# Kernel tuning notes

Measured on AMD Instinct MI355X. Metric: run time of the kernel, lower is better.

## Reference

```python
import math
import jax, jax.numpy as jnp
import numpy as np

B, C, NX, NY = 8, 16, 512, 512
N = 16384
N_RES, NH, S = 90, 5, 0.5


def _normal(x, mu, s):
    # exp(-0.5*((x-mu)/s)^2) / (sqrt(s^2) * sqrt(2*pi))  -- matches torch helper
    return jnp.exp(-0.5 * ((x - mu) / s) ** 2) / (jnp.sqrt(s * s) * math.sqrt(2.0 * math.pi))


def setup_inputs() -> dict:
    key = jax.random.key(0)
    k1, k2 = jax.random.split(key)
    x = jax.random.normal(k1, (B, C, NX, NY), dtype=jnp.float32)
    coords = jax.random.uniform(k2, (B, N, 2), dtype=jnp.float32)
    nh_m = (NH - 1) / 2 + 0.5
    pixel_offset_normal = jnp.linspace(nh_m, -nh_m, N_RES, dtype=jnp.float32)
    pixel_offset_indices = jnp.linspace(-(NH - 1) // 2, (NH - 1) // 2, NH, dtype=jnp.float32)
    s = jnp.float32(S)
    return {"x": x, "coords": coords, "s": s,
            "pixel_offset_normal": pixel_offset_normal,
            "pixel_offset_indices": pixel_offset_indices}


def reference(x, coords, s, pixel_offset_normal, pixel_offset_indices):
    b, n, _ = coords.shape
    _, c, nx, ny = x.shape
    nh = pixel_offset_indices.shape[0]

    # continuous positions in pixel space
    px = coords[:, :, 1] * (nx - 1)   # [b,n]
    py = coords[:, :, 0] * (ny - 1)
    rpx, rpy = jnp.round(px), jnp.round(py)

    # gaussian weights integrated over sub-pixel resolution (n_res samples -> nh bins)
    # NOTE: torch code clamps both axes with x.shape[-2] (=nx); replicated faithfully.
    pxo = jnp.clip(rpx[..., None] - pixel_offset_normal, 0.0, nx)   # [b,n,n_res]
    pyo = jnp.clip(rpy[..., None] - pixel_offset_normal, 0.0, nx)
    wx = _normal(pxo, px[..., None], s).reshape(b, n, nh, -1).sum(-1)  # [b,n,nh]
    wy = _normal(pyo, py[..., None], s).reshape(b, n, nh, -1).sum(-1)
    w2d = wx[..., :, None] * wy[..., None, :]                          # [b,n,nh,nh]
    w2d = w2d / w2d.reshape(b, n, -1).sum(-1)[..., None, None]

    # integer neighborhood indices (both axes clamped with nx-1, as in torch code)
    ix = jnp.clip(jnp.round(rpx[..., None] - pixel_offset_indices), 0, nx - 1).astype(jnp.int32)  # [b,n,nh]
    iy = jnp.clip(jnp.round(rpy[..., None] - pixel_offset_indices), 0, nx - 1).astype(jnp.int32)

    # per-batch gather of nh x nh neighborhoods (equivalent to torch's BxB gather + diagonal)
    flat = (ix[..., :, None] * ny + iy[..., None, :]).reshape(b, n * nh * nh)  # [b, n*nh*nh]
    xf = x.reshape(b, c, nx * ny)
    g = jax.vmap(lambda xi, idx: xi[:, idx])(xf, flat)       # [b,c,n*nh*nh]
    g = g.reshape(b, c, n, nh, nh)

    out = (g * w2d[:, None]).reshape(b, c, n, nh * nh).sum(-1)  # [b,c,n]
    return out
```

## Files before the change

kernel.cpp:

```cpp
#include <hip/hip_runtime.h>

#define BV    8
#define CV    16
#define NXV   512
#define NYV   512
#define NV    16384
#define NRES  90
#define NHV   5
#define TPB   256
#define CPERT 4

#define NPTS  (BV * NV)
#define TSH   3
#define TDIM  (NXV >> TSH)
#define NBUCKB (TDIM * TDIM)
#define NBUCK  (BV * NBUCKB)
#define SCANT 1024
#define SPT   (NBUCK / SCANT)

#if __has_builtin(__builtin_amdgcn_exp2f)
#define EXP2 __builtin_amdgcn_exp2f
#else
#define EXP2 exp2f
#endif

__global__ void zero_counts_kernel(int* __restrict__ counts) {
    int i = blockIdx.x * blockDim.x + threadIdx.x;
    if (i < NBUCK) counts[i] = 0;
}

__device__ __forceinline__ int bucket_key(float rpx, float rpy, int i) {
    const unsigned tx = ((unsigned)(int)rpx) >> TSH;
    const unsigned ty = ((unsigned)(int)rpy) >> TSH;
    unsigned m = 0;
    #pragma unroll
    for (int k = 0; k < 6; ++k)
        m |= (((tx >> k) & 1u) << (2 * k)) | (((ty >> k) & 1u) << (2 * k + 1));
    return (i >> 14) * NBUCKB + (int)m;
}

__global__ __launch_bounds__(TPB) void bucket_count_kernel(
    const float* __restrict__ coords, int* __restrict__ counts)
{
    const int i = blockIdx.x * TPB + threadIdx.x;
    const float2 cd = *(const float2*)(coords + (size_t)i * 2);
    const float rpx = rintf(cd.y * (float)(NXV - 1));
    const float rpy = rintf(cd.x * (float)(NYV - 1));
    atomicAdd(&counts[bucket_key(rpx, rpy, i)], 1);
}

__global__ __launch_bounds__(SCANT) void scan_kernel(
    const int* __restrict__ counts, int* __restrict__ cursors)
{
    __shared__ int sm[SCANT];
    const int tid  = threadIdx.x;
    const int base = tid * SPT;

    int v[SPT];
    int run = 0;
    #pragma unroll
    for (int k = 0; k < SPT; ++k) {
        v[k] = run;
        run += counts[base + k];
    }
    sm[tid] = run;
    __syncthreads();
    #pragma unroll
    for (int off = 1; off < SCANT; off <<= 1) {
        int t = sm[tid];
        if (tid >= off) t += sm[tid - off];
        __syncthreads();
        sm[tid] = t;
        __syncthreads();
    }
    const int tbase = sm[tid] - run;
    #pragma unroll
    for (int k = 0; k < SPT; ++k)
        cursors[base + k] = tbase + v[k];
}

__global__ __launch_bounds__(TPB) void scatter_weights_kernel(
    const float* __restrict__ coords,
    const float* __restrict__ s_ptr,
    const float* __restrict__ offn,
    const float* __restrict__ offi,
    int* __restrict__ cursors,
    float4* __restrict__ w8a, float4* __restrict__ w8b,
    float4* __restrict__ wx4, int4* __restrict__ off4,
    float4* __restrict__ misc)
{
    const int i = blockIdx.x * TPB + threadIdx.x;

    const float2 cd = *(const float2*)(coords + (size_t)i * 2);
    const float px  = cd.y * (float)(NXV - 1);
    const float py  = cd.x * (float)(NYV - 1);
    const float rpx = rintf(px);
    const float rpy = rintf(py);

    const int pos = atomicAdd(&cursors[bucket_key(rpx, rpy, i)], 1);

    const float s = s_ptr[0];
    const float k = -0.72134752044448169f / (s * s);

    float wx[NHV], wy[NHV];
    float sx = 0.f, sy = 0.f;
    #pragma unroll
    for (int h = 0; h < NHV; ++h) {
        float ax = 0.f, ay = 0.f;
        #pragma unroll 6
        for (int t = 0; t < NRES / NHV; ++t) {
            const float off = offn[h * (NRES / NHV) + t];
            const float vx = fminf(fmaxf(rpx - off, 0.f), (float)NXV);
            const float vy = fminf(fmaxf(rpy - off, 0.f), (float)NXV);
            const float dx = vx - px;
            const float dy = vy - py;
            ax += EXP2(k * dx * dx);
            ay += EXP2(k * dy * dy);
        }
        wx[h] = ax; wy[h] = ay;
        sx += ax;  sy += ay;
    }
    const float inv = 1.0f / (sx * sy);

    int ix[NHV], iy[NHV];
    #pragma unroll
    for (int h = 0; h < NHV; ++h) {
        const float fo = offi[h];
        ix[h] = (int)fminf(fmaxf(rintf(rpx - fo), 0.f), (float)(NXV - 1));
        iy[h] = (int)fminf(fmaxf(rintf(rpy - fo), 0.f), (float)(NXV - 1));
    }

    const int a = min(iy[NHV - 1] & ~3, NYV - 8);

    float w8[8];
    #pragma unroll
    for (int kk = 0; kk < 8; ++kk) {
        float w = 0.f;
        #pragma unroll
        for (int j = 0; j < NHV; ++j)
            w += (iy[j] - a == kk) ? wy[j] * inv : 0.f;
        w8[kk] = w;
    }

    w8a[pos] = make_float4(w8[0], w8[1], w8[2], w8[3]);
    w8b[pos] = make_float4(w8[4], w8[5], w8[6], w8[7]);
    wx4[pos] = make_float4(wx[0], wx[1], wx[2], wx[3]);
    off4[pos] = make_int4((ix[0] * NYV + a) * 4, (ix[1] * NYV + a) * 4,
                          (ix[2] * NYV + a) * 4, (ix[3] * NYV + a) * 4);
    misc[pos] = make_float4(wx[4], __int_as_float((ix[4] * NYV + a) * 4),
                            __int_as_float(i), 0.f);
}

__global__ __launch_bounds__(TPB, 4) void gather_kernel(
    const float* __restrict__ x,
    const float4* __restrict__ w8a, const float4* __restrict__ w8b,
    const float4* __restrict__ wx4, const int4* __restrict__ off4,
    const float4* __restrict__ misc,
    float* __restrict__ out)
{
    const int nwg = NPTS / TPB;
    const int bid = blockIdx.x;
    const int swz = (bid & 7) * (nwg / 8) + (bid >> 3);
    const int p   = swz * TPB + threadIdx.x;
    const int c0  = blockIdx.y * CPERT;

    const float4 wa = w8a[p];
    const float4 wb = w8b[p];
    const float4 wr = wx4[p];
    const int4   o4 = off4[p];
    const float4 ms = misc[p];
    const float  we = ms.x;
    const int    oe = __float_as_int(ms.y);
    const int    i  = __float_as_int(ms.z);
    const int    b  = i >> 14;
    const int    n  = i & (NV - 1);

    const int   ro[NHV] = {o4.x, o4.y, o4.z, o4.w, oe};
    const float rw[NHV] = {wr.x, wr.y, wr.z, wr.w, we};

    const char* base = (const char*)x + ((size_t)(b * CV + c0) << 20);
    float acc[CPERT];
    #pragma unroll
    for (int q = 0; q < CPERT; ++q) acc[q] = 0.f;

    #pragma unroll
    for (int q = 0; q < CPERT; ++q) {
        const char* bq = base + ((size_t)q << 20);
        #pragma unroll
        for (int r = 0; r < NHV; ++r) {
            const float4* rp = (const float4*)(bq + (size_t)(unsigned)ro[r]);
            const float4 va = rp[0];
            const float4 vb = rp[1];
            const float rs = va.x * wa.x + va.y * wa.y + va.z * wa.z +
                             va.w * wa.w + vb.x * wb.x + vb.y * wb.y +
                             vb.z * wb.z + vb.w * wb.w;
            acc[q] = fmaf(rw[r], rs, acc[q]);
        }
    }

    #pragma unroll
    for (int q = 0; q < CPERT; ++q)
        out[(((size_t)(b * CV + c0 + q)) << 14) + n] = acc[q];
}

extern "C" void kernel_launch(void* const* d_in, const int* in_sizes, int n_in,
                              void* d_out, int out_size, void* d_ws, size_t ws_size,
                              hipStream_t stream) {
    const float* x      = (const float*)d_in[0];
    const float* coords = (const float*)d_in[1];
    const float* s_ptr  = (const float*)d_in[2];
    const float* offn   = (const float*)d_in[3];
    const float* offi   = (const float*)d_in[4];
    float* out = (float*)d_out;

    char* w = (char*)d_ws;
    float4* w8a  = (float4*)w;  w += (size_t)NPTS * 16;
    float4* w8b  = (float4*)w;  w += (size_t)NPTS * 16;
    float4* wx4  = (float4*)w;  w += (size_t)NPTS * 16;
    int4*   off4 = (int4*)w;    w += (size_t)NPTS * 16;
    float4* misc = (float4*)w;  w += (size_t)NPTS * 16;
    int*    counts  = (int*)w;  w += (size_t)NBUCK * 4;
    int*    cursors = (int*)w;

    zero_counts_kernel<<<dim3(NBUCK / TPB), dim3(TPB), 0, stream>>>(counts);
    bucket_count_kernel<<<dim3(NPTS / TPB), dim3(TPB), 0, stream>>>(coords, counts);
    scan_kernel<<<dim3(1), dim3(SCANT), 0, stream>>>(counts, cursors);
    scatter_weights_kernel<<<dim3(NPTS / TPB), dim3(TPB), 0, stream>>>(
        coords, s_ptr, offn, offi, cursors, w8a, w8b, wx4, off4, misc);

    dim3 grid(NPTS / TPB, CV / CPERT, 1);
    gather_kernel<<<grid, dim3(TPB), 0, stream>>>(
        x, w8a, w8b, wx4, off4, misc, out);
}
```

Measured before the change: 287.9 us.

## Stage per-tile image patches in LDS and gather points from shared memory

Measured after the change: 262.2 us. -8.9%, faster.

```diff
diff --git a/kernel.cpp b/kernel.cpp
--- a/kernel.cpp
+++ b/kernel.cpp
@@ -8,16 +8,22 @@
 #define NRES  90
 #define NHV   5
 #define TPB   256
-#define CPERT 4
 
 #define NPTS  (BV * NV)
-#define TSH   3
+#define TSH   5
 #define TDIM  (NXV >> TSH)
 #define NBUCKB (TDIM * TDIM)
 #define NBUCK  (BV * NBUCKB)
 #define SCANT 1024
 #define SPT   (NBUCK / SCANT)
 
+#define CPG   4
+#define RROWS 36
+#define RCOLS 48
+#define RSEG  (RCOLS / 4)
+#define SLOTS_PER_CH (RROWS * RSEG)
+#define SLOTS (CPG * SLOTS_PER_CH)
+
 #if __has_builtin(__builtin_amdgcn_exp2f)
 #define EXP2 __builtin_amdgcn_exp2f
 #else
@@ -30,13 +36,9 @@
 }
 
 __device__ __forceinline__ int bucket_key(float rpx, float rpy, int i) {
-    const unsigned tx = ((unsigned)(int)rpx) >> TSH;
-    const unsigned ty = ((unsigned)(int)rpy) >> TSH;
-    unsigned m = 0;
-    #pragma unroll
-    for (int k = 0; k < 6; ++k)
-        m |= (((tx >> k) & 1u) << (2 * k)) | (((ty >> k) & 1u) << (2 * k + 1));
-    return (i >> 14) * NBUCKB + (int)m;
+    const int tr = ((int)rpx) >> TSH;
+    const int tc = ((int)rpy) >> TSH;
+    return (i >> 14) * NBUCKB + tr * TDIM + tc;
 }
 
 __global__ __launch_bounds__(TPB) void bucket_count_kernel(
@@ -50,7 +52,8 @@
 }
 
 __global__ __launch_bounds__(SCANT) void scan_kernel(
-    const int* __restrict__ counts, int* __restrict__ cursors)
+    const int* __restrict__ counts, int* __restrict__ starts,
+    int* __restrict__ cursors)
 {
     __shared__ int sm[SCANT];
     const int tid  = threadIdx.x;
@@ -75,8 +78,11 @@
     }
     const int tbase = sm[tid] - run;
     #pragma unroll
-    for (int k = 0; k < SPT; ++k)
-        cursors[base + k] = tbase + v[k];
+    for (int k = 0; k < SPT; ++k) {
+        const int e = tbase + v[k];
+        starts[base + k]  = e;
+        cursors[base + k] = e;
+    }
 }
 
 __global__ __launch_bounds__(TPB) void scatter_weights_kernel(
@@ -151,56 +157,81 @@
                             __int_as_float(i), 0.f);
 }
 
-__global__ __launch_bounds__(TPB, 4) void gather_kernel(
+__global__ __launch_bounds__(TPB) void tile_gather_kernel(
     const float* __restrict__ x,
+    const int* __restrict__ starts, const int* __restrict__ ends,
     const float4* __restrict__ w8a, const float4* __restrict__ w8b,
     const float4* __restrict__ wx4, const int4* __restrict__ off4,
     const float4* __restrict__ misc,
     float* __restrict__ out)
 {
-    const int nwg = NPTS / TPB;
+    __shared__ float4 lds[SLOTS];
+
     const int bid = blockIdx.x;
-    const int swz = (bid & 7) * (nwg / 8) + (bid >> 3);
-    const int p   = swz * TPB + threadIdx.x;
-    const int c0  = blockIdx.y * CPERT;
-
-    const float4 wa = w8a[p];
-    const float4 wb = w8b[p];
-    const float4 wr = wx4[p];
-    const int4   o4 = off4[p];
-    const float4 ms = misc[p];
-    const float  we = ms.x;
-    const int    oe = __float_as_int(ms.y);
-    const int    i  = __float_as_int(ms.z);
-    const int    b  = i >> 14;
-    const int    n  = i & (NV - 1);
-
-    const int   ro[NHV] = {o4.x, o4.y, o4.z, o4.w, oe};
-    const float rw[NHV] = {wr.x, wr.y, wr.z, wr.w, we};
-
-    const char* base = (const char*)x + ((size_t)(b * CV + c0) << 20);
-    float acc[CPERT];
-    #pragma unroll
-    for (int q = 0; q < CPERT; ++q) acc[q] = 0.f;
-
-    #pragma unroll
-    for (int q = 0; q < CPERT; ++q) {
-        const char* bq = base + ((size_t)q << 20);
-        #pragma unroll
-        for (int r = 0; r < NHV; ++r) {
-            const float4* rp = (const float4*)(bq + (size_t)(unsigned)ro[r]);
-            const float4 va = rp[0];
-            const float4 vb = rp[1];
-            const float rs = va.x * wa.x + va.y * wa.y + va.z * wa.z +
-                             va.w * wa.w + vb.x * wb.x + vb.y * wb.y +
-                             vb.z * wb.z + vb.w * wb.w;
-            acc[q] = fmaf(rw[r], rs, acc[q]);
+    const int cg  = blockIdx.y;
+    const int b   = bid >> 8;
+    const int tr  = (bid >> 4) & (TDIM - 1);
+    const int tc  = bid & (TDIM - 1);
+    const int r0  = tr << TSH, c0 = tc << TSH;
+    const int R0  = min(max(r0 - 2, 0), NXV - RROWS);
+    const int W0  = min(max(c0 - 8, 0), NYV - RCOLS);
+
+    const int tid = threadIdx.x;
+    const char* bx = (const char*)x + ((size_t)(b * CV + cg * CPG) << 20);
+
+    #pragma unroll
+    for (int kk = 0; kk < (SLOTS + TPB - 1) / TPB; ++kk) {
+        const int sslot = tid + kk * TPB;
+        if (sslot < SLOTS) {
+            const int ch  = sslot / SLOTS_PER_CH;
+            const int rem = sslot - ch * SLOTS_PER_CH;
+            const int row = rem / RSEG;
+            const int seg = rem - row * RSEG;
+            lds[sslot] = *(const float4*)(bx + ((size_t)ch << 20)
+                          + ((size_t)(R0 + row) << 11) + (W0 << 2) + (seg << 4));
         }
     }
-
-    #pragma unroll
-    for (int q = 0; q < CPERT; ++q)
-        out[(((size_t)(b * CV + c0 + q)) << 14) + n] = acc[q];
+    __syncthreads();
+
+    const int s0    = starts[bid];
+    const int total = (ends[bid] - s0) << 2;
+    const char* ldsb = (const char*)lds;
+
+    for (int item = tid; item < total; item += TPB) {
+        const int p  = s0 + (item >> 2);
+        const int ch = item & (CPG - 1);
+
+        const float4 wa = w8a[p];
+        const float4 wb = w8b[p];
+        const float4 wr = wx4[p];
+        const int4   o4 = off4[p];
+        const float4 ms = misc[p];
+        const float  we = ms.x;
+        const int    oe = __float_as_int(ms.y);
+        const int    i  = __float_as_int(ms.z);
+        const int    n  = i & (NV - 1);
+
+        const int basech = ch * (SLOTS_PER_CH * 16) - R0 * (RCOLS * 4) - (W0 << 2);
+
+        float acc = 0.f;
+#define ROW(OFF, WROW) {                                                     \
+        const int lo = basech + ((OFF) >> 11) * (RCOLS * 4) + ((OFF) & 2047);\
+        const float4 va = *(const float4*)(ldsb + lo);                       \
+        const float4 vb = *(const float4*)(ldsb + lo + 16);                  \
+        const float rs = va.x * wa.x + va.y * wa.y + va.z * wa.z +           \
+                         va.w * wa.w + vb.x * wb.x + vb.y * wb.y +           \
+                         vb.z * wb.z + vb.w * wb.w;                          \
+        acc = fmaf(WROW, rs, acc); }
+
+        ROW(o4.x, wr.x)
+        ROW(o4.y, wr.y)
+        ROW(o4.z, wr.z)
+        ROW(o4.w, wr.w)
+        ROW(oe,   we)
+#undef ROW
+
+        out[(((size_t)(b * CV + cg * CPG + ch)) << 14) + n] = acc;
+    }
 }
 
 extern "C" void kernel_launch(void* const* d_in, const int* in_sizes, int n_in,
@@ -220,15 +251,16 @@
     int4*   off4 = (int4*)w;    w += (size_t)NPTS * 16;
     float4* misc = (float4*)w;  w += (size_t)NPTS * 16;
     int*    counts  = (int*)w;  w += (size_t)NBUCK * 4;
+    int*    starts  = (int*)w;  w += (size_t)NBUCK * 4;
     int*    cursors = (int*)w;
 
     zero_counts_kernel<<<dim3(NBUCK / TPB), dim3(TPB), 0, stream>>>(counts);
     bucket_count_kernel<<<dim3(NPTS / TPB), dim3(TPB), 0, stream>>>(coords, counts);
-    scan_kernel<<<dim3(1), dim3(SCANT), 0, stream>>>(counts, cursors);
+    scan_kernel<<<dim3(1), dim3(SCANT), 0, stream>>>(counts, starts, cursors);
     scatter_weights_kernel<<<dim3(NPTS / TPB), dim3(TPB), 0, stream>>>(
         coords, s_ptr, offn, offi, cursors, w8a, w8b, wx4, off4, misc);
 
-    dim3 grid(NPTS / TPB, CV / CPERT, 1);
-    gather_kernel<<<grid, dim3(TPB), 0, stream>>>(
-        x, w8a, w8b, wx4, off4, misc, out);
-}
+    dim3 grid(NBUCK, CV / CPG, 1);
+    tile_gather_kernel<<<grid, dim3(TPB), 0, stream>>>(
+        x, starts, cursors, w8a, w8b, wx4, off4, misc, out);
+}
```
